# Performance work log

Measured on AMD Instinct MI355X. Metric: run time of the kernel, lower is better.

## Reference

```python
import jax, jax.numpy as jnp
import numpy as np

CH = 512
COND = 1280
HEADS = 8
GROUPS = CH // 8
EPS = 1e-5


def conv2d(x, w, b, pad):
    y = jax.lax.conv_general_dilated(
        x, w, window_strides=(1, 1), padding=[(pad, pad), (pad, pad)],
        dimension_numbers=('NCHW', 'OIHW', 'NCHW'))
    return y + b[None, :, None, None]


def group_norm(x, gamma, beta, groups, eps=EPS):
    b, c, h, w = x.shape
    xg = x.reshape(b, groups, c // groups, h, w)
    mu = xg.mean(axis=(2, 3, 4), keepdims=True)
    var = xg.var(axis=(2, 3, 4), keepdims=True)
    xn = ((xg - mu) * jax.lax.rsqrt(var + eps)).reshape(b, c, h, w)
    return xn * gamma[None, :, None, None] + beta[None, :, None, None]


def setup_inputs() -> dict:
    key = jax.random.key(0)
    ks = jax.random.split(key, 20)
    s = 0.05
    inp = {
        'x': jax.random.normal(ks[0], (8, CH, 32, 32), jnp.float32),
        'conditioning': jax.random.normal(ks[1], (8, COND), jnp.float32),
        # ResBlock params
        'c1w': jax.random.normal(ks[2], (CH, CH, 3, 3), jnp.float32) * s,
        'c1b': jnp.zeros((CH,), jnp.float32),
        'g1w': jnp.ones((CH,), jnp.float32),
        'g1b': jnp.zeros((CH,), jnp.float32),
        'c2w': jax.random.normal(ks[3], (CH, CH, 3, 3), jnp.float32) * s,
        'c2b': jnp.zeros((CH,), jnp.float32),
        'g2w': jnp.ones((CH,), jnp.float32),
        'g2b': jnp.zeros((CH,), jnp.float32),
        'cpw': jax.random.normal(ks[4], (CH, COND), jnp.float32) * s,
        'cpb': jnp.zeros((CH,), jnp.float32),
        'rpw': jax.random.normal(ks[5], (CH, CH, 1, 1), jnp.float32) * s,
        'rpb': jnp.zeros((CH,), jnp.float32),
        # Attention params (1x1 convs)
        'qw': jax.random.normal(ks[6], (CH, CH, 1, 1), jnp.float32) * s,
        'qb': jnp.zeros((CH,), jnp.float32),
        'kw': jax.random.normal(ks[7], (CH, CH, 1, 1), jnp.float32) * s,
        'kb': jnp.zeros((CH,), jnp.float32),
        'vw': jax.random.normal(ks[8], (CH, CH, 1, 1), jnp.float32) * s,
        'vb': jnp.zeros((CH,), jnp.float32),
        'ow': jax.random.normal(ks[9], (CH, CH, 1, 1), jnp.float32) * s,
        'ob': jnp.zeros((CH,), jnp.float32),
    }
    return inp


def reference(x, conditioning, c1w, c1b, g1w, g1b, c2w, c2b, g2w, g2b,
              cpw, cpb, rpw, rpb, qw, qb, kw, kb, vw, vb, ow, ob):
    # --- ResBlock ---
    residual = conv2d(x, rpw, rpb, 0)
    h = conv2d(x, c1w, c1b, 1)
    h = group_norm(h, g1w, g1b, GROUPS)
    h = jax.nn.silu(h)
    h = conv2d(h, c2w, c2b, 1)
    h = group_norm(h, g2w, g2b, GROUPS)
    cond = conditioning @ cpw.T + cpb  # [B, C]
    h = h * (1.0 + cond[:, :, None, None]) + residual

    # --- SpatialSelfAttention ---
    b, c, hh, ww = h.shape
    d = c // HEADS
    scale = d ** (-0.5)
    q = conv2d(h, qw, qb, 0).reshape(b, HEADS, d, hh * ww)
    k = conv2d(h, kw, kb, 0).reshape(b, HEADS, d, hh * ww)
    v = conv2d(h, vw, vb, 0).reshape(b, HEADS, d, hh * ww)
    attn = jnp.einsum('bhdn,bhdm->bhnm', q, k) * scale  # [B,H,N,N]
    attn = jax.nn.softmax(attn, axis=-1)
    out = jnp.einsum('bhnm,bhdm->bhdn', attn, v).reshape(b, c, hh, ww)
    return conv2d(out, ow, ob, 0) + h
```

## Files before the change

### kernel.cpp

```cpp
#include <hip/hip_runtime.h>
#include <hip/hip_bf16.h>

typedef unsigned short u16;
typedef unsigned long long u64;
typedef __attribute__((ext_vector_type(8))) short bf8;
typedef __attribute__((ext_vector_type(4))) short bf4;
typedef __attribute__((ext_vector_type(4))) float f32x4;

#define CH_ 512
#define NSP 1024
#define NB 8
#define CONDDIM 1280
#define NGROUP 64
#define HEADS_ 8
#define HD 64
#define PR 34
#define PPB (PR*PR)
#define QSCALE 0.18033688011112042f

#define VWAIT(N) asm volatile("s_waitcnt vmcnt(" #N ")" ::: "memory")
#define SCHEDB __builtin_amdgcn_sched_barrier(0)
#define BARRIER do { SCHEDB; __builtin_amdgcn_s_barrier(); SCHEDB; } while (0)

__device__ __forceinline__ u16 f2bf(float f) {
  union { float f; unsigned u; } v; v.f = f;
  unsigned u = v.u;
  return (u16)((u + 0x7fffu + ((u >> 16) & 1u)) >> 16);
}

__device__ __forceinline__ float b2f(u16 x) {
  union { unsigned u; float f; } v; v.u = ((unsigned)x) << 16; return v.f;
}

__device__ __forceinline__ unsigned cvt_pk_bf16(float lo, float hi) {
  unsigned r;
  asm volatile("v_cvt_pk_bf16_f32 %0, %1, %2" : "=v"(r) : "v"(lo), "v"(hi));
  return r;
}

__device__ __forceinline__ f32x4 mfma_bf16(bf8 a, bf8 b, f32x4 c) {
  return __builtin_amdgcn_mfma_f32_16x16x32_bf16(a, b, c, 0, 0, 0);
}

__device__ __forceinline__ void gload16(const void* g, void* l) {
  __builtin_amdgcn_global_load_lds((const __attribute__((address_space(1))) void*)g,
                                   (__attribute__((address_space(3))) void*)l, 16, 0, 0);
}

__global__ __launch_bounds__(256) void prep_kernel(
    const float* __restrict__ x, u16* __restrict__ xp, u16* __restrict__ h1p,
    const float* __restrict__ c1w, const float* __restrict__ c2w,
    u16* __restrict__ w1p, u16* __restrict__ w2p,
    const float* __restrict__ rpw, const float* __restrict__ qw, const float* __restrict__ kw,
    const float* __restrict__ vw, const float* __restrict__ ow,
    u16* __restrict__ wrp, u16* __restrict__ wq, u16* __restrict__ wk,
    u16* __restrict__ wv, u16* __restrict__ wo,
    const float* __restrict__ cd, const float* __restrict__ cpw,
    const float* __restrict__ cpb, float* __restrict__ cond) {
  __shared__ float t[32][33];
  int bid = blockIdx.x;
  int tid = threadIdx.x;
  if (bid < 4096) {
    int px = bid & 31, py = (bid >> 5) & 15, b = bid >> 9;
    int c0 = py * 32, p0 = px * 32;
    int tx = tid & 31, ty = tid >> 5;
#pragma unroll
    for (int i = 0; i < 4; i++) {
      int row = ty + i * 8;
      t[row][tx] = x[((size_t)b * CH_ + c0 + row) * NSP + p0 + tx];
    }
    __syncthreads();
#pragma unroll
    for (int i = 0; i < 4; i++) {
      int pr = ty + i * 8;
      int p = p0 + pr;
      int y = p >> 5, xc = p & 31;
      xp[((size_t)b * PPB + (size_t)(y + 1) * PR + xc + 1) * CH_ + c0 + tx] = f2bf(t[tx][pr]);
    }
  } else if (bid < 4360) {
    int id = (bid - 4096) * 256 + tid;
    int ch8 = id & 63;
    int rest = id >> 6;
    int bidx = rest % 132;
    int bb = rest / 132;
    int r, c;
    if (bidx < 34)       { r = 0;          c = bidx; }
    else if (bidx < 68)  { r = 33;         c = bidx - 34; }
    else if (bidx < 100) { r = bidx - 67;  c = 0; }
    else                 { r = bidx - 99;  c = 33; }
    size_t off = ((size_t)bb * PPB + (size_t)r * PR + c) * CH_ + ch8 * 8;
    const bf8 z = {0, 0, 0, 0, 0, 0, 0, 0};
    *(bf8*)(xp + off) = z;
    *(bf8*)(h1p + off) = z;
  } else if (bid < 6664) {
    int id2 = bid - 4360;
    int which = (id2 >= 1152) ? 1 : 0;
    int id = (id2 - which * 1152) * 256 + tid;
    const float* w = which ? c2w : c1w;
    u16* wp = which ? w2p : w1p;
    int co = id & (CH_ - 1);
    int cib = (id >> 9) & 63;
    int tt = id >> 15;
    int dy = tt / 3, dx = tt % 3;
    bf8 v;
#pragma unroll
    for (int j = 0; j < 8; j++) {
      int ci = cib * 8 + j;
      v[j] = (short)f2bf(w[(((size_t)co * CH_ + ci) * 3 + dy) * 3 + dx]);
    }
    *(bf8*)(wp + ((size_t)(tt * 64 + cib) * CH_ + co) * 8) = v;
  } else if (bid < 7304) {
    int id3 = bid - 6664;
    int which = id3 >> 7;
    int id = (id3 & 127) * 256 + tid;
    const float* w; u16* wp;
    switch (which) {
      case 0: w = rpw; wp = wrp; break;
      case 1: w = qw;  wp = wq;  break;
      case 2: w = kw;  wp = wk;  break;
      case 3: w = vw;  wp = wv;  break;
      default: w = ow; wp = wo;  break;
    }
    int co = id & (CH_ - 1);
    int cib = id >> 9;
    bf8 v;
#pragma unroll
    for (int j = 0; j < 8; j++) v[j] = (short)f2bf(w[(size_t)co * CH_ + cib * 8 + j]);
    *(bf8*)(wp + ((size_t)cib * CH_ + co) * 8) = v;
  } else {
    int id4 = bid - 7304;
    int b = id4 >> 7;
    int c = (id4 & 127) * 4 + (tid >> 6);
    int lane = tid & 63;
    const float* wrow = cpw + (size_t)c * CONDDIM;
    const float* crow = cd + (size_t)b * CONDDIM;
    float s = 0.f;
    for (int i = lane; i < CONDDIM; i += 64) s += crow[i] * wrow[i];
#pragma unroll
    for (int m = 32; m > 0; m >>= 1) s += __shfl_xor(s, m, 64);
    if (lane == 0) cond[b * CH_ + c] = s + cpb[c];
  }
}

template <int TAPS, int PIN, int EPI>
__global__ __launch_bounds__(256, 3) void conv_kernel(
    const u16* __restrict__ in, const u16* __restrict__ wp, const float* __restrict__ bias,
    float* __restrict__ outf, const float* __restrict__ addf,
    u16* __restrict__ o0, u16* __restrict__ o1, u16* __restrict__ o2,
    const float* __restrict__ b0, const float* __restrict__ b1, const float* __restrict__ b2,
    const u16* __restrict__ wp2, float* __restrict__ outf2, const float* __restrict__ bias2) {
  constexpr int LDSZ = (TAPS == 9) ? (2 * 14336 + 3 * 12288 + (EPI == 8 ? 2 * 4096 : 0))
                                   : (4 * 8192 + 4 * 4096);
  __shared__ char lds[LDSZ];
  char* ldsA = lds;
  char* ldsB = lds + ((TAPS == 9) ? 2 * 14336 : 4 * 8192);
  char* ldsR = lds + 2 * 14336 + 3 * 12288;

  const int b = blockIdx.z;
  int seg = 0, coy = blockIdx.y;
  if constexpr (EPI == 5) { seg = coy >> 3; coy &= 7; }
  const int co0 = coy * 64;
  const int p0 = blockIdx.x * 128;
  const int tid = threadIdx.x;
  const int lane = tid & 63, wid = tid >> 6;
  const int wv = wid >> 1, wc = wid & 1;
  const int l15 = lane & 15, lhi = lane >> 4;

  const char* aSrc;
  if constexpr (TAPS == 9) {
    aSrc = (const char*)in + ((size_t)b * PPB + (size_t)blockIdx.x * 4 * PR) * 1024;
  } else if constexpr (PIN) {
    aSrc = (const char*)in + (size_t)b * PPB * 1024;
  } else {
    aSrc = (const char*)in + ((size_t)b * NSP + p0) * 1024;
  }
  const char* bSrc = (const char*)wp + (size_t)((EPI == 5) ? seg * 524288 : 0) + co0 * 16;
  const char* rSrc = (const char*)wp2 + co0 * 16;

  const int pB = ((tid >> 6) * 512 + (tid & 63)) * 16;
  int pA0, pA1, pA3 = 0;
  if constexpr (TAPS == 9) {
    int r0 = tid >> 2;
    int c0s = (tid & 3) ^ ((r0 >> 1) & 3);
    pA0 = (r0 << 10) + (c0s << 4);
    int r3 = 192 + ((tid & 127) >> 2);
    int c3s = (tid & 3) ^ ((r3 >> 1) & 3);
    pA3 = (r3 << 10) + (c3s << 4);
    pA1 = 0;
  } else {
    int a0 = (tid >> 2), a1 = 64 + (tid >> 2);
    int cs = (tid & 3) ^ (((tid >> 2) >> 1) & 3);
    if constexpr (PIN) {
      int pp0 = p0 + a0, pp1 = p0 + a1;
      int g0 = ((pp0 >> 5) + 1) * PR + (pp0 & 31) + 1;
      int g1 = ((pp1 >> 5) + 1) * PR + (pp1 & 31) + 1;
      pA0 = (g0 << 10) + (cs << 4);
      pA1 = (g1 << 10) + (cs << 4);
    } else {
      pA0 = (a0 << 10) + (cs << 4);
      pA1 = (a1 << 10) + (cs << 4);
    }
  }

  const int rowbA = (TAPS == 9) ? (wv * 68 + l15) : (wv * 64 + l15);
  const int aAddr = rowbA * 64 + ((lhi ^ ((l15 >> 1) & 3)) << 4);
  const int bAddr = (lhi * 64 + wc * 32 + l15) * 16;

  f32x4 acc[4][2], accR[4][2];
#pragma unroll
  for (int m = 0; m < 4; m++)
#pragma unroll
    for (int n = 0; n < 2; n++) { acc[m][n] = {0.f, 0.f, 0.f, 0.f}; accR[m][n] = {0.f, 0.f, 0.f, 0.f}; }

  if constexpr (TAPS == 9) {
    gload16(aSrc + pA0,          ldsA + (wid << 10));
    gload16(aSrc + pA0 + 65536,  ldsA + 4096 + (wid << 10));
    gload16(aSrc + pA0 + 131072, ldsA + 8192 + (wid << 10));
    gload16(aSrc + pA3,          ldsA + 12288 + ((wid & 1) << 10));
    gload16(bSrc + (size_t)(0 * 64) * 8192 + pB, ldsB + (wid << 10));
    gload16(bSrc + (size_t)(1 * 64) * 8192 + pB, ldsB + 4096 + (wid << 10));
    gload16(bSrc + (size_t)(2 * 64) * 8192 + pB, ldsB + 8192 + (wid << 10));
    gload16(bSrc + (size_t)(3 * 64) * 8192 + pB, ldsB + 12288 + (wid << 10));
    gload16(bSrc + (size_t)(4 * 64) * 8192 + pB, ldsB + 12288 + 4096 + (wid << 10));
    gload16(bSrc + (size_t)(5 * 64) * 8192 + pB, ldsB + 12288 + 8192 + (wid << 10));
    if constexpr (EPI == 8) {
      gload16(rSrc + pB, ldsR + (wid << 10));
      VWAIT(4);
    } else {
      VWAIT(3);
    }
    BARRIER;

#define AREAD(Ab_, K) (*(const bf8*)((Ab_) + (rowbA + (K)) * 64 + ((lhi ^ (((rowbA + (K)) >> 1) & 3)) << 4)))

#define PH3(KC, T, AS) do {                                                             \
    const int kcn_ = ((KC) < 15) ? (KC) + 1 : 15;                                       \
    if constexpr ((T) == 0) {                                                           \
      gload16(bSrc + (size_t)(6 * 64 + (KC) * 4) * 8192 + pB, ldsB + 24576 + (wid << 10)); \
      gload16(bSrc + (size_t)(7 * 64 + (KC) * 4) * 8192 + pB, ldsB + 24576 + 4096 + (wid << 10)); \
      gload16(bSrc + (size_t)(8 * 64 + (KC) * 4) * 8192 + pB, ldsB + 24576 + 8192 + (wid << 10)); \
      gload16(aSrc + kcn_ * 64 + pA0,         ldsA + (1 - (AS)) * 14336 + (wid << 10)); \
      gload16(aSrc + kcn_ * 64 + pA0 + 65536, ldsA + (1 - (AS)) * 14336 + 4096 + (wid << 10)); \
    } else if constexpr ((T) == 1) {                                                    \
      gload16(bSrc + (size_t)(0 * 64 + kcn_ * 4) * 8192 + pB, ldsB + (wid << 10));      \
      gload16(bSrc + (size_t)(1 * 64 + kcn_ * 4) * 8192 + pB, ldsB + 4096 + (wid << 10)); \
      gload16(bSrc + (size_t)(2 * 64 + kcn_ * 4) * 8192 + pB, ldsB + 8192 + (wid << 10)); \
      gload16(aSrc + kcn_ * 64 + pA0 + 131072, ldsA + (1 - (AS)) * 14336 + 8192 + (wid << 10)); \
      if constexpr (EPI == 8)                                                           \
        if ((KC) < 15)                                                                  \
          gload16(rSrc + (size_t)kcn_ * 32768 + pB, ldsR + (kcn_ & 1) * 4096 + (wid << 10)); \
    } else {                                                                            \
      gload16(bSrc + (size_t)(3 * 64 + kcn_ * 4) * 8192 + pB, ldsB + 12288 + (wid << 10)); \
      gload16(bSrc + (size_t)(4 * 64 + kcn_ * 4) * 8192 + pB, ldsB + 12288 + 4096 + (wid << 10)); \
      gload16(bSrc + (size_t)(5 * 64 + kcn_ * 4) * 8192 + pB, ldsB + 12288 + 8192 + (wid << 10)); \
      gload16(aSrc + kcn_ * 64 + pA3, ldsA + (1 - (AS)) * 14336 + 12288 + ((wid & 1) << 10)); \
    }                                                                                   \
    SCHEDB;                                                                             \
    {                                                                                   \
      const char* Ab_ = ldsA + (AS) * 14336;                                            \
      const char* Bb_ = ldsB + (T) * 12288;                                             \
      bf8 af_[3][4], bq_[3][2];                                                         \
      _Pragma("unroll")                                                                 \
      for (int tt = 0; tt < 3; tt++) {                                                  \
        const int DT_ = (T) * 34 + tt;                                                  \
        af_[tt][0] = AREAD(Ab_, DT_ + 0);                                               \
        af_[tt][1] = AREAD(Ab_, DT_ + 16);                                              \
        af_[tt][2] = AREAD(Ab_, DT_ + 34);                                              \
        af_[tt][3] = AREAD(Ab_, DT_ + 50);                                              \
        bq_[tt][0] = *(const bf8*)(Bb_ + tt * 4096 + 0   + bAddr);                      \
        bq_[tt][1] = *(const bf8*)(Bb_ + tt * 4096 + 256 + bAddr);                      \
      }                                                                                 \
      __builtin_amdgcn_s_setprio(1);                                                    \
      _Pragma("unroll")                                                                 \
      for (int tt = 0; tt < 3; tt++)                                                    \
        _Pragma("unroll")                                                               \
        for (int m = 0; m < 4; m++) {                                                   \
          acc[m][0] = mfma_bf16(af_[tt][m], bq_[tt][0], acc[m][0]);                     \
          acc[m][1] = mfma_bf16(af_[tt][m], bq_[tt][1], acc[m][1]);                     \
        }                                                                               \
      if constexpr (EPI == 8 && (T) == 1) {                                             \
        bf8 rq0 = *(const bf8*)(ldsR + ((KC) & 1) * 4096 + 0   + bAddr);                \
        bf8 rq1 = *(const bf8*)(ldsR + ((KC) & 1) * 4096 + 256 + bAddr);                \
        _Pragma("unroll")                                                               \
        for (int m = 0; m < 4; m++) {                                                   \
          accR[m][0] = mfma_bf16(af_[1][m], rq0, accR[m][0]);                           \
          accR[m][1] = mfma_bf16(af_[1][m], rq1, accR[m][1]);                           \
        }                                                                               \
      }                                                                                 \
      __builtin_amdgcn_s_setprio(0);                                                    \
    }                                                                                   \
    if constexpr ((T) == 0) { VWAIT(5); }                                               \
    else if constexpr ((T) == 1) {                                                      \
      if constexpr (EPI == 8) { VWAIT(5); } else { VWAIT(4); }                          \
    } else { VWAIT(4); }                                                                \
    BARRIER;                                                                            \
  } while (0)

    for (int kc2 = 0; kc2 < 8; kc2++) {
      PH3(kc2 * 2,     0, 0); PH3(kc2 * 2,     1, 0); PH3(kc2 * 2,     2, 0);
      PH3(kc2 * 2 + 1, 0, 1); PH3(kc2 * 2 + 1, 1, 1); PH3(kc2 * 2 + 1, 2, 1);
    }
#undef PH3
#undef AREAD
  } else {
    gload16(aSrc + pA0,         ldsA + (wid << 10));
    gload16(aSrc + pA1,         ldsA + 4096 + (wid << 10));
    gload16(bSrc + pB,          ldsB + (wid << 10));
    gload16(aSrc + 64 + pA0,    ldsA + 8192 + (wid << 10));
    gload16(aSrc + 64 + pA1,    ldsA + 8192 + 4096 + (wid << 10));
    gload16(bSrc + 32768 + pB,  ldsB + 4096 + (wid << 10));
    VWAIT(3);
    BARRIER;

#define PH1(KC, S) do {                                                                 \
    constexpr int S2 = ((S) + 2) & 3;                                                   \
    const int kcn_ = ((KC) + 2 < 16) ? (KC) + 2 : 15;                                   \
    gload16(bSrc + (size_t)kcn_ * 32768 + pB, ldsB + S2 * 4096 + (wid << 10));          \
    gload16(aSrc + kcn_ * 64 + pA0, ldsA + S2 * 8192 + (wid << 10));                    \
    gload16(aSrc + kcn_ * 64 + pA1, ldsA + S2 * 8192 + 4096 + (wid << 10));             \
    SCHEDB;                                                                             \
    bf8 af0 = *(const bf8*)(ldsA + (S) * 8192 + 0    + aAddr);                          \
    bf8 af1 = *(const bf8*)(ldsA + (S) * 8192 + 1024 + aAddr);                          \
    bf8 af2 = *(const bf8*)(ldsA + (S) * 8192 + 2048 + aAddr);                          \
    bf8 af3 = *(const bf8*)(ldsA + (S) * 8192 + 3072 + aAddr);                          \
    bf8 bq0 = *(const bf8*)(ldsB + (S) * 4096 + 0   + bAddr);                           \
    bf8 bq1 = *(const bf8*)(ldsB + (S) * 4096 + 256 + bAddr);                           \
    __builtin_amdgcn_s_setprio(1);                                                      \
    acc[0][0] = mfma_bf16(af0, bq0, acc[0][0]);                                         \
    acc[0][1] = mfma_bf16(af0, bq1, acc[0][1]);                                         \
    acc[1][0] = mfma_bf16(af1, bq0, acc[1][0]);                                         \
    acc[1][1] = mfma_bf16(af1, bq1, acc[1][1]);                                         \
    acc[2][0] = mfma_bf16(af2, bq0, acc[2][0]);                                         \
    acc[2][1] = mfma_bf16(af2, bq1, acc[2][1]);                                         \
    acc[3][0] = mfma_bf16(af3, bq0, acc[3][0]);                                         \
    acc[3][1] = mfma_bf16(af3, bq1, acc[3][1]);                                         \
    __builtin_amdgcn_s_setprio(0);                                                      \
    VWAIT(3);                                                                           \
    BARRIER;                                                                            \
  } while (0)

    for (int kc4 = 0; kc4 < 4; kc4++) {
      PH1(kc4 * 4 + 0, 0); PH1(kc4 * 4 + 1, 1); PH1(kc4 * 4 + 2, 2); PH1(kc4 * 4 + 3, 3);
    }
#undef PH1
  }

  VWAIT(0);

#pragma unroll
  for (int m = 0; m < 4; m++) {
    int pbase = p0 + wv * 64 + m * 16 + lhi * 4;
#pragma unroll
    for (int n = 0; n < 2; n++) {
      int co = co0 + wc * 32 + n * 16 + l15;
      if constexpr (EPI == 7) {
        float bv = bias[co];
#pragma unroll
        for (int r = 0; r < 4; r++)
          o0[((size_t)b * NSP + pbase + r) * CH_ + co] = f2bf(acc[m][n][r] + bv);
      } else if constexpr (EPI == 8) {
        float bv = bias[co];
        float rv = bias2[co];
#pragma unroll
        for (int r = 0; r < 4; r++) {
          size_t idx = ((size_t)b * NSP + pbase + r) * CH_ + co;
          o0[idx]    = f2bf(acc[m][n][r] + bv);
          outf2[idx] = accR[m][n][r] + rv;
        }
      } else if constexpr (EPI == 2) {
        float bv = bias[co];
        f32x4 v;
#pragma unroll
        for (int r = 0; r < 4; r++)
          v[r] = acc[m][n][r] + bv + addf[((size_t)b * NSP + pbase + r) * CH_ + co];
        *(f32x4*)(outf + ((size_t)b * CH_ + co) * NSP + pbase) = v;
      } else {
        if (seg == 0) {
          float bv = b0[co];
#pragma unroll
          for (int r = 0; r < 4; r++)
            o0[((size_t)b * NSP + pbase + r) * CH_ + co] = f2bf((acc[m][n][r] + bv) * QSCALE);
        } else if (seg == 1) {
          float bv = b1[co];
#pragma unroll
          for (int r = 0; r < 4; r++)
            o1[((size_t)b * NSP + pbase + r) * CH_ + co] = f2bf(acc[m][n][r] + bv);
        } else {
          float bv = b2[co];
          union { bf4 v; u64 u; } pk4;
#pragma unroll
          for (int r = 0; r < 4; r++) pk4.v[r] = (short)f2bf(acc[m][n][r] + bv);
          int np = (pbase & ~31) | ((pbase & 12) << 1) | ((pbase & 16) >> 2);
          *(u64*)(o2 + ((size_t)b * CH_ + co) * NSP + np) = pk4.u;
        }
      }
    }
  }
}

template <int MODE>
__global__ __launch_bounds__(256) void gn_kernel(
    const u16* __restrict__ in, const float* __restrict__ gw, const float* __restrict__ gb,
    const float* __restrict__ cond, const float* __restrict__ resid,
    float* __restrict__ outf, u16* __restrict__ outb) {
  int b = blockIdx.y, g = blockIdx.x;
  int tid = threadIdx.x;
  const u16* base = in + (size_t)b * NSP * CH_ + g * 8;
  bf8 v[4];
  float s = 0.f, ss = 0.f;
#pragma unroll
  for (int i = 0; i < 4; i++) {
    int p = tid + i * 256;
    v[i] = *(const bf8*)(base + (size_t)p * CH_);
#pragma unroll
    for (int j = 0; j < 8; j++) { float f = b2f((u16)v[i][j]); s += f; ss += f * f; }
  }
  __shared__ float rs[256], rss[256];
  rs[tid] = s; rss[tid] = ss;
  __syncthreads();
  for (int off = 128; off > 0; off >>= 1) {
    if (tid < off) { rs[tid] += rs[tid + off]; rss[tid] += rss[tid + off]; }
    __syncthreads();
  }
  float mean = rs[0] * (1.f / 8192.f);
  float var = rss[0] * (1.f / 8192.f) - mean * mean;
  float inv = rsqrtf(var + 1e-5f);
  float gam[8], bet[8], cm[8];
  *(f32x4*)(gam)     = *(const f32x4*)(gw + g * 8);
  *(f32x4*)(gam + 4) = *(const f32x4*)(gw + g * 8 + 4);
  *(f32x4*)(bet)     = *(const f32x4*)(gb + g * 8);
  *(f32x4*)(bet + 4) = *(const f32x4*)(gb + g * 8 + 4);
  if (MODE == 1) {
    *(f32x4*)(cm)     = *(const f32x4*)(cond + b * CH_ + g * 8);
    *(f32x4*)(cm + 4) = *(const f32x4*)(cond + b * CH_ + g * 8 + 4);
#pragma unroll
    for (int j = 0; j < 8; j++) cm[j] += 1.f;
  }
#pragma unroll
  for (int i = 0; i < 4; i++) {
    int p = tid + i * 256;
    if (MODE == 0) {
      bf8 ov;
#pragma unroll
      for (int j = 0; j < 8; j++) {
        float y = (b2f((u16)v[i][j]) - mean) * inv * gam[j] + bet[j];
        float sg = 1.f / (1.f + __expf(-y));
        ov[j] = (short)f2bf(y * sg);
      }
      int yy = p >> 5, xc = p & 31;
      *(bf8*)(outb + ((size_t)b * PPB + (size_t)(yy + 1) * PR + xc + 1) * CH_ + g * 8) = ov;
    } else {
      size_t idx = ((size_t)b * NSP + p) * CH_ + g * 8;
      f32x4 r0 = *(const f32x4*)(resid + idx);
      f32x4 r1 = *(const f32x4*)(resid + idx + 4);
      f32x4 z0, z1; bf8 ov;
#pragma unroll
      for (int j = 0; j < 4; j++) {
        float y = (b2f((u16)v[i][j]) - mean) * inv * gam[j] + bet[j];
        z0[j] = y * cm[j] + r0[j];
        ov[j] = (short)f2bf(z0[j]);
      }
#pragma unroll
      for (int j = 0; j < 4; j++) {
        float y = (b2f((u16)v[i][4 + j]) - mean) * inv * gam[4 + j] + bet[4 + j];
        z1[j] = y * cm[4 + j] + r1[j];
        ov[4 + j] = (short)f2bf(z1[j]);
      }
      *(f32x4*)(outf + idx)     = z0;
      *(f32x4*)(outf + idx + 4) = z1;
      *(bf8*)(outb + idx) = ov;
    }
  }
}

__global__ __launch_bounds__(256, 2) void attn_kernel(const u16* __restrict__ q, const u16* __restrict__ k,
                                                      const u16* __restrict__ vT, u16* __restrict__ ao) {
  int bid = blockIdx.x;
  int swz = (bid & 7) * 64 + (bid >> 3);
  int b = swz >> 6;
  int head = (swz >> 3) & 7;
  int qt = swz & 7;
  int tid = threadIdx.x, lane = tid & 63, wid = tid >> 6;
  int l15 = lane & 15, lhi = lane >> 4;
  int cb = head * HD;
  int q0 = qt * 128 + wid * 32;

  const char* qp = (const char*)(q + (size_t)b * NSP * CH_ + cb);
  const char* kp = (const char*)(k + (size_t)b * NSP * CH_ + cb);
  const char* vp = (const char*)(vT + ((size_t)b * CH_ + cb) * NSP);

  __shared__ u16 Ksh[3][64 * 64];
  __shared__ u16 Vsh[3][64 * 64];

  bf8 aq[2][2];
#pragma unroll
  for (int qh = 0; qh < 2; qh++)
#pragma unroll
    for (int ks = 0; ks < 2; ks++)
      aq[qh][ks] = *(const bf8*)(qp + ((size_t)(q0 + qh * 16 + l15) * CH_ + ks * 32 + lhi * 8) * 2);

  const bf8 ones8 = {16256, 16256, 16256, 16256, 16256, 16256, 16256, 16256};

  f32x4 o[2][4], osum[2];
#pragma unroll
  for (int qh = 0; qh < 2; qh++) {
    osum[qh] = {0.f, 0.f, 0.f, 0.f};
#pragma unroll
    for (int n = 0; n < 4; n++) o[qh][n] = {0.f, 0.f, 0.f, 0.f};
  }

  auto stage = [&](int kt, int buf) {
#pragma unroll
    for (int t = 0; t < 2; t++) {
      int i = wid * 2 + t;
      int chunk = i * 64 + lane;
      int r = chunk >> 3, c = chunk & 7;
      gload16(kp + (size_t)(kt * 64 + r) * 1024 + (size_t)((c ^ (r & 7)) * 16),
              (char*)Ksh[buf] + i * 1024);
    }
#pragma unroll
    for (int t = 0; t < 2; t++) {
      int i = wid * 2 + t;
      int chunk = i * 64 + lane;
      int r = chunk >> 3, c = chunk & 7;
      gload16(vp + (size_t)r * 2048 + (size_t)(kt * 128) + (size_t)((c ^ (r & 7)) * 16),
              (char*)Vsh[buf] + i * 1024);
    }
  };

  auto qk = [&](int buf, f32x4 (&sacc)[2][4]) {
    const char* Kb = (const char*)Ksh[0] + buf * 8192;
#pragma unroll
    for (int qh = 0; qh < 2; qh++)
#pragma unroll
      for (int kf = 0; kf < 4; kf++) sacc[qh][kf] = {0.f, 0.f, 0.f, 0.f};
#pragma unroll
    for (int kf = 0; kf < 4; kf++) {
      bf8 ak[2];
#pragma unroll
      for (int ks = 0; ks < 2; ks++)
        ak[ks] = *(const bf8*)(Kb + (size_t)(kf * 16 + l15) * 128 + (((ks * 4 + lhi) ^ (l15 & 7)) * 16));
#pragma unroll
      for (int qh = 0; qh < 2; qh++)
#pragma unroll
        for (int ks = 0; ks < 2; ks++)
          sacc[qh][kf] = mfma_bf16(ak[ks], aq[qh][ks], sacc[qh][kf]);
    }
  };

  auto smpv = [&](int buf, f32x4 (&sacc)[2][4]) {
    const char* Vb = (const char*)Vsh[0] + buf * 8192;
    unsigned pk[2][4][2];
#pragma unroll
    for (int qh = 0; qh < 2; qh++)
#pragma unroll
      for (int kf = 0; kf < 4; kf++) {
        f32x4 pv;
#pragma unroll
        for (int r = 0; r < 4; r++) pv[r] = exp2f(sacc[qh][kf][r]);
        pk[qh][kf][0] = cvt_pk_bf16(pv[0], pv[1]);
        pk[qh][kf][1] = cvt_pk_bf16(pv[2], pv[3]);
      }
#pragma unroll
    for (int g = 0; g < 2; g++) {
      union { bf8 v8; unsigned u[4]; } ap[2];
#pragma unroll
      for (int qh = 0; qh < 2; qh++) {
        ap[qh].u[0] = pk[qh][2 * g][0];
        ap[qh].u[1] = pk[qh][2 * g][1];
        ap[qh].u[2] = pk[qh][2 * g + 1][0];
        ap[qh].u[3] = pk[qh][2 * g + 1][1];
      }
#pragma unroll
      for (int nf2 = 0; nf2 < 4; nf2++) {
        int row = nf2 * 16 + l15;
        bf8 bv8 = *(const bf8*)(Vb + (size_t)row * 128 + (((4 * g + lhi) ^ (l15 & 7)) * 16));
#pragma unroll
        for (int qh = 0; qh < 2; qh++)
          o[qh][nf2] = mfma_bf16(ap[qh].v8, bv8, o[qh][nf2]);
      }
#pragma unroll
      for (int qh = 0; qh < 2; qh++)
        osum[qh] = mfma_bf16(ap[qh].v8, ones8, osum[qh]);
    }
  };

  stage(0, 0);
  stage(1, 1);
  VWAIT(4);
  BARRIER;

  f32x4 saccA[2][4], saccB[2][4];
  qk(0, saccA);

  int bc = 0;
  for (int kt2 = 0; kt2 < 8; kt2++) {
    {
      int kt = 2 * kt2;
      int bn = (bc == 2) ? 0 : bc + 1;
      int bs = (bn == 2) ? 0 : bn + 1;
      VWAIT(0);
      BARRIER;
      qk(bn, saccB);
      if (kt < 14) stage(kt + 2, bs);
      smpv(bc, saccA);
      bc = bn;
    }
    {
      int kt = 2 * kt2 + 1;
      if (kt < 15) {
        int bn = (bc == 2) ? 0 : bc + 1;
        int bs = (bn == 2) ? 0 : bn + 1;
        VWAIT(0);
        BARRIER;
        qk(bn, saccA);
        if (kt < 14) stage(kt + 2, bs);
        smpv(bc, saccB);
        bc = bn;
      } else {
        smpv(bc, saccB);
      }
    }
  }

#pragma unroll
  for (int qh = 0; qh < 2; qh++) {
    float linv[4];
#pragma unroll
    for (int r = 0; r < 4; r++) linv[r] = 1.f / osum[qh][r];
#pragma unroll
    for (int nf2 = 0; nf2 < 4; nf2++)
#pragma unroll
      for (int r = 0; r < 4; r++) {
        float val = o[qh][nf2][r] * linv[r];
        ao[((size_t)b * NSP + q0 + qh * 16 + lhi * 4 + r) * CH_ + cb + nf2 * 16 + l15] = f2bf(val);
      }
  }
}


extern "C" void kernel_launch(void* const* d_in, const int* in_sizes, int n_in,
                              void* d_out, int out_size, void* d_ws, size_t ws_size,
                              hipStream_t stream) {
  const float* x    = (const float*)d_in[0];
  const float* cnd  = (const float*)d_in[1];
  const float* c1w  = (const float*)d_in[2];
  const float* c1b  = (const float*)d_in[3];
  const float* g1w  = (const float*)d_in[4];
  const float* g1b  = (const float*)d_in[5];
  const float* c2w  = (const float*)d_in[6];
  const float* c2b  = (const float*)d_in[7];
  const float* g2w  = (const float*)d_in[8];
  const float* g2b  = (const float*)d_in[9];
  const float* cpw  = (const float*)d_in[10];
  const float* cpb  = (const float*)d_in[11];
  const float* rpw  = (const float*)d_in[12];
  const float* rpb  = (const float*)d_in[13];
  const float* qw   = (const float*)d_in[14];
  const float* qb   = (const float*)d_in[15];
  const float* kw   = (const float*)d_in[16];
  const float* kb   = (const float*)d_in[17];
  const float* vw   = (const float*)d_in[18];
  const float* vb   = (const float*)d_in[19];
  const float* ow   = (const float*)d_in[20];
  const float* ob   = (const float*)d_in[21];
  float* out = (float*)d_out;

  char* ws = (char*)d_ws;
  size_t off = 0;
  auto alloc = [&](size_t bytes) -> char* {
    char* p = ws + off;
    off = (off + bytes + 255) & ~(size_t)255;
    return p;
  };
  const size_t ACT_F = (size_t)NB * NSP * CH_ * 4;
  const size_t ACT_B = (size_t)NB * NSP * CH_ * 2;
  const size_t PAD_B = (size_t)NB * PPB * CH_ * 2;

  u16* xp    = (u16*)alloc(PAD_B);
  u16* h1p   = (u16*)alloc(PAD_B);
  u16* w1p   = (u16*)alloc((size_t)9 * CH_ * CH_ * 2);
  u16* w2p   = (u16*)alloc((size_t)9 * CH_ * CH_ * 2);
  u16* wrp   = (u16*)alloc((size_t)CH_ * CH_ * 2);
  u16* wqkv  = (u16*)alloc((size_t)3 * CH_ * CH_ * 2);
  u16* wop   = (u16*)alloc((size_t)CH_ * CH_ * 2);
  float* cndv = (float*)alloc((size_t)NB * CH_ * 4);
  float* resid = (float*)alloc(ACT_F);
  float* h12  = (float*)alloc(ACT_F);
  u16* hb    = (u16*)alloc(ACT_B);
  u16* qbuf  = (u16*)alloc(ACT_B);
  u16* kbuf  = (u16*)alloc(ACT_B);
  u16* vTb   = (u16*)alloc(ACT_B);
  u16* aob   = (u16*)alloc(ACT_B);
  if (off > ws_size) return;

  u16* actb = aob;

  prep_kernel<<<8328, 256, 0, stream>>>(x, xp, h1p, c1w, c2w, w1p, w2p,
                                        rpw, qw, kw, vw, ow,
                                        wrp, wqkv, wqkv + (size_t)CH_ * CH_,
                                        wqkv + (size_t)2 * CH_ * CH_, wop,
                                        cnd, cpw, cpb, cndv);

  dim3 ggrid(NSP / 128, CH_ / 64, NB);
  dim3 qgrid(NSP / 128, 3 * CH_ / 64, NB);
  conv_kernel<9, 1, 8><<<ggrid, 256, 0, stream>>>(xp, w1p, c1b, nullptr, nullptr,
                                                  actb, nullptr, nullptr, nullptr, nullptr, nullptr,
                                                  wrp, resid, rpb);
  gn_kernel<0><<<dim3(NGROUP, NB), 256, 0, stream>>>(actb, g1w, g1b, nullptr, nullptr, nullptr, h1p);
  conv_kernel<9, 1, 7><<<ggrid, 256, 0, stream>>>(h1p, w2p, c2b, nullptr, nullptr,
                                                  actb, nullptr, nullptr, nullptr, nullptr, nullptr,
                                                  nullptr, nullptr, nullptr);
  gn_kernel<1><<<dim3(NGROUP, NB), 256, 0, stream>>>(actb, g2w, g2b, cndv, resid, h12, hb);
  conv_kernel<1, 0, 5><<<qgrid, 256, 0, stream>>>(hb, wqkv, nullptr, nullptr, nullptr,
                                                  qbuf, kbuf, vTb, qb, kb, vb,
                                                  nullptr, nullptr, nullptr);
  attn_kernel<<<512, 256, 0, stream>>>(qbuf, kbuf, vTb, aob);
  conv_kernel<1, 0, 2><<<ggrid, 256, 0, stream>>>(aob, wop, ob, out, h12,
                                                  nullptr, nullptr, nullptr, nullptr, nullptr, nullptr,
                                                  nullptr, nullptr, nullptr);
}
```

Before: 221.3 us.

## Shrink LDS staging buffers to raise occupancy in conv kernels

```diff
diff --git a/kernel.cpp b/kernel.cpp
--- a/kernel.cpp
+++ b/kernel.cpp
@@ -143,18 +143,18 @@
 }
 
 template <int TAPS, int PIN, int EPI>
-__global__ __launch_bounds__(256, 3) void conv_kernel(
+__global__ __launch_bounds__(256, TAPS == 9 ? 3 : 4) void conv_kernel(
     const u16* __restrict__ in, const u16* __restrict__ wp, const float* __restrict__ bias,
     float* __restrict__ outf, const float* __restrict__ addf,
     u16* __restrict__ o0, u16* __restrict__ o1, u16* __restrict__ o2,
     const float* __restrict__ b0, const float* __restrict__ b1, const float* __restrict__ b2,
     const u16* __restrict__ wp2, float* __restrict__ outf2, const float* __restrict__ bias2) {
-  constexpr int LDSZ = (TAPS == 9) ? (2 * 14336 + 3 * 12288 + (EPI == 8 ? 2 * 4096 : 0))
-                                   : (4 * 8192 + 4 * 4096);
+  constexpr int LDSZ = (TAPS == 9) ? (2 * 14336 + 2 * 12288 + (EPI == 8 ? 2 * 4096 : 0))
+                                   : (3 * 8192 + 3 * 4096);
   __shared__ char lds[LDSZ];
   char* ldsA = lds;
-  char* ldsB = lds + ((TAPS == 9) ? 2 * 14336 : 4 * 8192);
-  char* ldsR = lds + 2 * 14336 + 3 * 12288;
+  char* ldsB = lds + ((TAPS == 9) ? 2 * 14336 : 3 * 8192);
+  char* ldsR = lds + 2 * 14336 + 2 * 12288;
 
   const int b = blockIdx.z;
   int seg = 0, coy = blockIdx.y;
@@ -220,45 +220,37 @@
     gload16(bSrc + (size_t)(0 * 64) * 8192 + pB, ldsB + (wid << 10));
     gload16(bSrc + (size_t)(1 * 64) * 8192 + pB, ldsB + 4096 + (wid << 10));
     gload16(bSrc + (size_t)(2 * 64) * 8192 + pB, ldsB + 8192 + (wid << 10));
-    gload16(bSrc + (size_t)(3 * 64) * 8192 + pB, ldsB + 12288 + (wid << 10));
-    gload16(bSrc + (size_t)(4 * 64) * 8192 + pB, ldsB + 12288 + 4096 + (wid << 10));
-    gload16(bSrc + (size_t)(5 * 64) * 8192 + pB, ldsB + 12288 + 8192 + (wid << 10));
-    if constexpr (EPI == 8) {
-      gload16(rSrc + pB, ldsR + (wid << 10));
-      VWAIT(4);
-    } else {
-      VWAIT(3);
-    }
+    if constexpr (EPI == 8) gload16(rSrc + pB, ldsR + (wid << 10));
+    VWAIT(0);
     BARRIER;
 
 #define AREAD(Ab_, K) (*(const bf8*)((Ab_) + (rowbA + (K)) * 64 + ((lhi ^ (((rowbA + (K)) >> 1) & 3)) << 4)))
 
-#define PH3(KC, T, AS) do {                                                             \
+#define PH3(KC, T, AS, H) do {                                                          \
     const int kcn_ = ((KC) < 15) ? (KC) + 1 : 15;                                       \
+    { const int kb_ = ((T) == 2) ? kcn_ : (KC);                                         \
+      const int tn_ = 3 * (((T) + 1) % 3);                                              \
+      gload16(bSrc + (size_t)((tn_ + 0) * 64 + kb_ * 4) * 8192 + pB,                    \
+              ldsB + (1 - (H)) * 12288 + (wid << 10));                                  \
+      gload16(bSrc + (size_t)((tn_ + 1) * 64 + kb_ * 4) * 8192 + pB,                    \
+              ldsB + (1 - (H)) * 12288 + 4096 + (wid << 10));                           \
+      gload16(bSrc + (size_t)((tn_ + 2) * 64 + kb_ * 4) * 8192 + pB,                    \
+              ldsB + (1 - (H)) * 12288 + 8192 + (wid << 10)); }                         \
     if constexpr ((T) == 0) {                                                           \
-      gload16(bSrc + (size_t)(6 * 64 + (KC) * 4) * 8192 + pB, ldsB + 24576 + (wid << 10)); \
-      gload16(bSrc + (size_t)(7 * 64 + (KC) * 4) * 8192 + pB, ldsB + 24576 + 4096 + (wid << 10)); \
-      gload16(bSrc + (size_t)(8 * 64 + (KC) * 4) * 8192 + pB, ldsB + 24576 + 8192 + (wid << 10)); \
       gload16(aSrc + kcn_ * 64 + pA0,         ldsA + (1 - (AS)) * 14336 + (wid << 10)); \
       gload16(aSrc + kcn_ * 64 + pA0 + 65536, ldsA + (1 - (AS)) * 14336 + 4096 + (wid << 10)); \
     } else if constexpr ((T) == 1) {                                                    \
-      gload16(bSrc + (size_t)(0 * 64 + kcn_ * 4) * 8192 + pB, ldsB + (wid << 10));      \
-      gload16(bSrc + (size_t)(1 * 64 + kcn_ * 4) * 8192 + pB, ldsB + 4096 + (wid << 10)); \
-      gload16(bSrc + (size_t)(2 * 64 + kcn_ * 4) * 8192 + pB, ldsB + 8192 + (wid << 10)); \
       gload16(aSrc + kcn_ * 64 + pA0 + 131072, ldsA + (1 - (AS)) * 14336 + 8192 + (wid << 10)); \
       if constexpr (EPI == 8)                                                           \
         if ((KC) < 15)                                                                  \
           gload16(rSrc + (size_t)kcn_ * 32768 + pB, ldsR + (kcn_ & 1) * 4096 + (wid << 10)); \
     } else {                                                                            \
-      gload16(bSrc + (size_t)(3 * 64 + kcn_ * 4) * 8192 + pB, ldsB + 12288 + (wid << 10)); \
-      gload16(bSrc + (size_t)(4 * 64 + kcn_ * 4) * 8192 + pB, ldsB + 12288 + 4096 + (wid << 10)); \
-      gload16(bSrc + (size_t)(5 * 64 + kcn_ * 4) * 8192 + pB, ldsB + 12288 + 8192 + (wid << 10)); \
       gload16(aSrc + kcn_ * 64 + pA3, ldsA + (1 - (AS)) * 14336 + 12288 + ((wid & 1) << 10)); \
     }                                                                                   \
     SCHEDB;                                                                             \
     {                                                                                   \
       const char* Ab_ = ldsA + (AS) * 14336;                                            \
-      const char* Bb_ = ldsB + (T) * 12288;                                             \
+      const char* Bb_ = ldsB + (H) * 12288;                                             \
       bf8 af_[3][4], bq_[3][2];                                                         \
       _Pragma("unroll")                                                                 \
       for (int tt = 0; tt < 3; tt++) {                                                  \
@@ -289,16 +281,16 @@
       }                                                                                 \
       __builtin_amdgcn_s_setprio(0);                                                    \
     }                                                                                   \
-    if constexpr ((T) == 0) { VWAIT(5); }                                               \
+    if constexpr ((T) == 0) { VWAIT(2); }                                               \
     else if constexpr ((T) == 1) {                                                      \
-      if constexpr (EPI == 8) { VWAIT(5); } else { VWAIT(4); }                          \
-    } else { VWAIT(4); }                                                                \
+      if constexpr (EPI == 8) { VWAIT(2); } else { VWAIT(1); }                          \
+    } else { VWAIT(1); }                                                                \
     BARRIER;                                                                            \
   } while (0)
 
     for (int kc2 = 0; kc2 < 8; kc2++) {
-      PH3(kc2 * 2,     0, 0); PH3(kc2 * 2,     1, 0); PH3(kc2 * 2,     2, 0);
-      PH3(kc2 * 2 + 1, 0, 1); PH3(kc2 * 2 + 1, 1, 1); PH3(kc2 * 2 + 1, 2, 1);
+      PH3(kc2 * 2,     0, 0, 0); PH3(kc2 * 2,     1, 0, 1); PH3(kc2 * 2,     2, 0, 0);
+      PH3(kc2 * 2 + 1, 0, 1, 1); PH3(kc2 * 2 + 1, 1, 1, 0); PH3(kc2 * 2 + 1, 2, 1, 1);
     }
 #undef PH3
 #undef AREAD
@@ -313,7 +305,7 @@
     BARRIER;
 
 #define PH1(KC, S) do {                                                                 \
-    constexpr int S2 = ((S) + 2) & 3;                                                   \
+    constexpr int S2 = ((S) + 2) % 3;                                                   \
     const int kcn_ = ((KC) + 2 < 16) ? (KC) + 2 : 15;                                   \
     gload16(bSrc + (size_t)kcn_ * 32768 + pB, ldsB + S2 * 4096 + (wid << 10));          \
     gload16(aSrc + kcn_ * 64 + pA0, ldsA + S2 * 8192 + (wid << 10));                    \
@@ -339,9 +331,10 @@
     BARRIER;                                                                            \
   } while (0)
 
-    for (int kc4 = 0; kc4 < 4; kc4++) {
-      PH1(kc4 * 4 + 0, 0); PH1(kc4 * 4 + 1, 1); PH1(kc4 * 4 + 2, 2); PH1(kc4 * 4 + 3, 3);
-    }
+    PH1(0, 0);  PH1(1, 1);  PH1(2, 2);  PH1(3, 0);
+    PH1(4, 1);  PH1(5, 2);  PH1(6, 0);  PH1(7, 1);
+    PH1(8, 2);  PH1(9, 0);  PH1(10, 1); PH1(11, 2);
+    PH1(12, 0); PH1(13, 1); PH1(14, 2); PH1(15, 0);
 #undef PH1
   }
 
```

Measured after the change: 221.0 us, median of 2. About the same (-0.2%).
